# Kernel optimization log

Measured on AMD Instinct MI355X. Metric: run time of the kernel, lower is better.

The kernel has to match this reference:

```python
import jax, jax.numpy as jnp
import numpy as np

N = 50000
E = 640000
H = 128
C = 3

def _xavier(key, shape, gain=1.0):
    fan_in, fan_out = shape[0], shape[1]
    a = gain * np.sqrt(6.0 / (fan_in + fan_out))
    return jax.random.uniform(key, shape, jnp.float32, -a, a)

def setup_inputs() -> dict:
    key = jax.random.key(0)
    ks = jax.random.split(key, 12)
    h = jax.random.normal(ks[0], (N, H), jnp.float32)
    x = jax.random.normal(ks[1], (N, C), jnp.float32)
    edge_index = jax.random.randint(ks[2], (2, E), 0, N, jnp.int64 if jax.config.jax_enable_x64 else jnp.int32)
    # edge_mlp: Linear(2H+1 -> H), SiLU, Linear(H -> H), SiLU
    We1 = _xavier(ks[3], (2 * H + 1, H)); be1 = jnp.zeros((H,), jnp.float32)
    We2 = _xavier(ks[4], (H, H));          be2 = jnp.zeros((H,), jnp.float32)
    # coord_mlp: Linear(H -> H), SiLU, Linear(H -> 1, no bias, gain 0.01)
    Wc1 = _xavier(ks[5], (H, H)); bc1 = jnp.zeros((H,), jnp.float32)
    Wc2 = _xavier(ks[6], (H, 1), gain=0.01)
    # node_mlp: Linear(2H -> H), SiLU, Linear(H -> H)
    Wn1 = _xavier(ks[7], (2 * H, H)); bn1 = jnp.zeros((H,), jnp.float32)
    Wn2 = _xavier(ks[8], (H, H));     bn2 = jnp.zeros((H,), jnp.float32)
    return dict(h=h, x=x, edge_index=edge_index,
                We1=We1, be1=be1, We2=We2, be2=be2,
                Wc1=Wc1, bc1=bc1, Wc2=Wc2,
                Wn1=Wn1, bn1=bn1, Wn2=Wn2, bn2=bn2)

def reference(h, x, edge_index, We1, be1, We2, be2, Wc1, bc1, Wc2, Wn1, bn1, Wn2, bn2):
    src, dst = edge_index[0], edge_index[1]
    n = h.shape[0]
    rel_pos = x[src] - x[dst]                              # [E, C]
    dist_sq = jnp.sum(rel_pos * rel_pos, axis=-1, keepdims=True)  # [E, 1]
    edge_input = jnp.concatenate([h[src], h[dst], dist_sq], axis=-1)  # [E, 2H+1]
    m_ij = jax.nn.silu(edge_input @ We1 + be1)
    m_ij = jax.nn.silu(m_ij @ We2 + be2)                   # [E, H]
    coord_weight = jax.nn.silu(m_ij @ Wc1 + bc1) @ Wc2     # [E, 1]
    coord_agg = jax.ops.segment_sum(rel_pos * coord_weight, dst, num_segments=n)
    x_out = x + coord_agg
    msg_agg = jax.ops.segment_sum(m_ij, dst, num_segments=n)  # [N, H]
    node_input = jnp.concatenate([h, msg_agg], axis=-1)    # [N, 2H]
    h_upd = jax.nn.silu(node_input @ Wn1 + bn1) @ Wn2 + bn2
    h_out = h + h_upd
    return (h_out, x_out)
```

## Files before the change

### kernel.cpp

```cpp
#include <hip/hip_runtime.h>

#define H 128

typedef __bf16 bf8_t __attribute__((ext_vector_type(8)));
typedef float  f4_t  __attribute__((ext_vector_type(4)));

#define MFMA16(a, b, c) __builtin_amdgcn_mfma_f32_16x16x32_bf16((a), (b), (c), 0, 0, 0)

__device__ __forceinline__ float silu_f(float v) {
    return v * (1.0f / (1.0f + __expf(-v)));
}

__device__ __forceinline__ void bar_lds() {
    asm volatile("s_waitcnt lgkmcnt(0)\ns_barrier" ::: "memory");
}

__device__ __forceinline__ float wload(const void* p, int idx, bool f32) {
    return f32 ? ((const float*)p)[idx] : (float)((const __bf16*)p)[idx];
}

__device__ __forceinline__ bf8_t hload8(const void* p, size_t off, bool f32) {
    bf8_t v;
    if (f32) {
        const float4* q = (const float4*)((const float*)p + off);
        const float4 a = q[0], b = q[1];
        v[0]=(__bf16)a.x; v[1]=(__bf16)a.y; v[2]=(__bf16)a.z; v[3]=(__bf16)a.w;
        v[4]=(__bf16)b.x; v[5]=(__bf16)b.y; v[6]=(__bf16)b.z; v[7]=(__bf16)b.w;
    } else {
        v = *(const bf8_t*)((const __bf16*)p + off);
    }
    return v;
}

__device__ __forceinline__ int eidx(const void* ei, int i, bool i64) {
    return i64 ? (int)((const long long*)ei)[i] : ((const int*)ei)[i];
}

__global__ void detect_kernel(const unsigned short* __restrict__ hraw,
                              const int* __restrict__ eiraw, int* __restrict__ flags)
{
    __shared__ int s_nf, s_oddnz;
    if (threadIdx.x == 0) { s_nf = 0; s_oddnz = 0; }
    __syncthreads();
    int nf = 0;
    for (int i = threadIdx.x; i < 16384; i += blockDim.x) {
        const unsigned short u = hraw[i];
        if (((u >> 7) & 0xFF) == 0xFF) nf++;
    }
    int onz = 0;
    for (int i = threadIdx.x; i < 512; i += blockDim.x) {
        if (eiraw[2*i + 1] != 0) onz++;
    }
    if (nf)  atomicAdd(&s_nf, nf);
    if (onz) atomicAdd(&s_oddnz, onz);
    __syncthreads();
    if (threadIdx.x == 0) {
        flags[0] = (s_nf > 0) ? 1 : 0;
        flags[1] = (s_oddnz == 0) ? 1 : 0;
    }
}

__global__ void histd_kernel(const void* __restrict__ ei, int* __restrict__ cnt,
                             const int* __restrict__ flags, int Ee)
{
    const int e = blockIdx.x*blockDim.x + threadIdx.x;
    if (e < Ee) atomicAdd(&cnt[eidx(ei, Ee + e, flags[1] != 0)], 1);
}

__global__ void scanA_kernel(const int* __restrict__ cnt, int* __restrict__ bsum, int Nn)
{
    __shared__ int s[512];
    const int gi = blockIdx.x*512 + threadIdx.x;
    s[threadIdx.x] = (gi < Nn) ? cnt[gi] : 0;
    __syncthreads();
    for (int off = 256; off > 0; off >>= 1) {
        if (threadIdx.x < off) s[threadIdx.x] += s[threadIdx.x + off];
        __syncthreads();
    }
    if (threadIdx.x == 0) bsum[blockIdx.x] = s[0];
}

__global__ void scanB_kernel(int* __restrict__ bsum, int* __restrict__ base, int nCh)
{
    if (threadIdx.x == 0) {
        int acc = 0;
        for (int b = 0; b < nCh; ++b) { base[b] = acc; acc += bsum[b]; }
    }
}

__global__ void scanC_kernel(const int* __restrict__ cnt, const int* __restrict__ base,
                             int* __restrict__ off, int* __restrict__ cursor, int Nn)
{
    __shared__ int s[512];
    const int i  = threadIdx.x;
    const int gi = blockIdx.x*512 + i;
    const int v  = (gi < Nn) ? cnt[gi] : 0;
    s[i] = v;
    __syncthreads();
    for (int o = 1; o < 512; o <<= 1) {
        const int t = (i >= o) ? s[i - o] : 0;
        __syncthreads();
        s[i] += t;
        __syncthreads();
    }
    const int excl = s[i] - v;
    if (gi <= Nn) {
        const int val = base[blockIdx.x] + excl;
        off[gi] = val;
        if (gi < Nn) cursor[gi] = val;
    }
}

__global__ void scatgeo_kernel(const void* __restrict__ ei, int* __restrict__ cursor,
                               int* __restrict__ srcs, int* __restrict__ dsts,
                               float4* __restrict__ rel4, const void* __restrict__ x,
                               const int* __restrict__ flags, int Ee)
{
    const int e = blockIdx.x*blockDim.x + threadIdx.x;
    if (e >= Ee) return;
    const bool i64 = flags[1] != 0;
    const bool f32 = flags[0] != 0;
    const int s = eidx(ei, e, i64);
    const int d = eidx(ei, Ee + e, i64);
    const int p = atomicAdd(&cursor[d], 1);
    srcs[p] = s;
    dsts[p] = d;
    float r[3];
    #pragma unroll
    for (int c = 0; c < 3; ++c)
        r[c] = wload(x, s*3 + c, f32) - wload(x, d*3 + c, f32);
    float4 o; o.x = r[0]; o.y = r[1]; o.z = r[2];
    o.w = r[0]*r[0] + r[1]*r[1] + r[2]*r[2];
    rel4[p] = o;
}

__global__ __launch_bounds__(512, 2)
void proj_kernel(const void* __restrict__ h, const void* __restrict__ We1,
                 const void* __restrict__ be1, const int* __restrict__ flags,
                 __bf16* __restrict__ PB, int Nn)
{
    const bool f32 = flags[0] != 0;
    const int tid  = threadIdx.x;
    const int wv   = tid >> 6;
    const int lane = tid & 63;
    const int quad = lane >> 4;
    const int l15  = lane & 15;

    bf8_t bW[4][2];
    float bias[2];
    #pragma unroll
    for (int t = 0; t < 2; ++t) {
        const int n    = wv*32 + t*16 + l15;
        const int rb   = (n < 128) ? 0 : 128;
        const int col  = n & 127;
        #pragma unroll
        for (int kc = 0; kc < 4; ++kc) {
            bf8_t v;
            #pragma unroll
            for (int j = 0; j < 8; ++j)
                v[j] = (__bf16)wload(We1, (rb + kc*32 + quad*8 + j)*H + col, f32);
            bW[kc][t] = v;
        }
        bias[t] = (n < 128) ? 0.f : wload(be1, col, f32);
    }

    __shared__ __bf16 s_h[32*136];

    const int tiles = (Nn + 31) >> 5;
    for (int tile = blockIdx.x; tile < tiles; tile += gridDim.x) {
        const int nb = tile << 5;
        __syncthreads();
        {
            const int m = tid >> 4, c = tid & 15;
            int node = nb + m; if (node >= Nn) node = Nn - 1;
            *(bf8_t*)&s_h[m*136 + c*8] = hload8(h, (size_t)node*H + c*8, f32);
        }
        __syncthreads();

        f4_t acc[2][2];
        #pragma unroll
        for (int mm = 0; mm < 2; ++mm)
            #pragma unroll
            for (int t = 0; t < 2; ++t) acc[mm][t] = (f4_t){0.f,0.f,0.f,0.f};
        #pragma unroll
        for (int kc = 0; kc < 4; ++kc) {
            #pragma unroll
            for (int mm = 0; mm < 2; ++mm) {
                const bf8_t a = *(const bf8_t*)&s_h[(mm*16 + l15)*136 + quad*8 + kc*32];
                acc[mm][0] = MFMA16(a, bW[kc][0], acc[mm][0]);
                acc[mm][1] = MFMA16(a, bW[kc][1], acc[mm][1]);
            }
        }
        #pragma unroll
        for (int mm = 0; mm < 2; ++mm)
            #pragma unroll
            for (int i = 0; i < 4; ++i) {
                const int row = nb + mm*16 + quad*4 + i;
                if (row < Nn) {
                    #pragma unroll
                    for (int t = 0; t < 2; ++t)
                        PB[(size_t)row*256 + wv*32 + t*16 + l15] =
                            (__bf16)(acc[mm][t][i] + bias[t]);
                }
            }
    }
}

__global__ __launch_bounds__(512, 2)
void egnn_edge_pipe_kernel(const __bf16* __restrict__ PB,
                           const int* __restrict__ srcs, const int* __restrict__ dsts,
                           const float4* __restrict__ rel4,
                           const void* __restrict__ We1,
                           const void* __restrict__ We2, const void* __restrict__ be2,
                           const void* __restrict__ Wc1, const void* __restrict__ bc1,
                           const void* __restrict__ Wc2, const int* __restrict__ flags,
                           float* __restrict__ msg, float* __restrict__ coord,
                           int Ee)
{
    const bool f32 = flags[0] != 0;
    const int tid  = threadIdx.x;
    const int wv   = tid >> 6;
    const int lane = tid & 63;
    const int quad = lane >> 4;
    const int l15  = lane & 15;
    const int mg   = wv >> 2;
    const int ng   = wv & 3;

    bf8_t bW2[4][2], bWc[4][2];
    float be2v[2], bc1v[2], wc2v[2];
    #pragma unroll
    for (int t = 0; t < 2; ++t) {
        const int n = ng*32 + t*16 + l15;
        #pragma unroll
        for (int kc = 0; kc < 4; ++kc) {
            bf8_t v, u;
            #pragma unroll
            for (int j = 0; j < 8; ++j) {
                v[j] = (__bf16)wload(We2, (kc*32 + quad*8 + j)*H + n, f32);
                u[j] = (__bf16)wload(Wc1, (kc*32 + quad*8 + j)*H + n, f32);
            }
            bW2[kc][t] = v;
            bWc[kc][t] = u;
        }
        be2v[t] = wload(be2, n, f32);
        bc1v[t] = wload(bc1, n, f32);
        wc2v[t] = wload(Wc2, n, f32);
    }

    const int em = tid >> 3;
    const int ch = tid & 7;
    float w1dA[8], w1dB[8];
    #pragma unroll
    for (int j = 0; j < 8; ++j) {
        w1dA[j] = wload(We1, 256*H + ch*8 + j, f32);
        w1dB[j] = wload(We1, 256*H + (ch+8)*8 + j, f32);
    }

    const int rcol = tid >> 2;
    const int rg   = tid & 3;
    const int qb   = lane & ~3;

    __shared__ __bf16 s_m1[64*136];
    __shared__ __bf16 s_m2[64*136];
    __shared__ float  s_cw[4*64];
    __shared__ int    s_dst[2][64];
    __shared__ float4 s_rl[2][64];

    const int tiles = (Ee + 63) >> 6;
    const float* rw = (const float*)rel4;

    bf8_t rA0, rA1, rB0, rB1;
    float d2cur, d2nxt;
    int   s_n, d_n, d_c;
    float4 r4c, r4n;
    {
        int e0 = blockIdx.x*64 + em; if (e0 >= Ee) e0 = Ee - 1;
        const int sc = srcs[e0], dc = dsts[e0];
        d_c = dc;
        d2cur = rw[(size_t)e0*4 + 3];
        if (ch == 0) r4c = rel4[e0];
        rA0 = *(const bf8_t*)(PB + (size_t)sc*256 + ch*8);
        rA1 = *(const bf8_t*)(PB + (size_t)sc*256 + (ch+8)*8);
        rB0 = *(const bf8_t*)(PB + (size_t)dc*256 + 128 + ch*8);
        rB1 = *(const bf8_t*)(PB + (size_t)dc*256 + 128 + (ch+8)*8);
        const int t1 = blockIdx.x + gridDim.x;
        const int tt = (t1 < tiles) ? t1 : blockIdx.x;
        int e1 = tt*64 + em; if (e1 >= Ee) e1 = Ee - 1;
        s_n = srcs[e1]; d_n = dsts[e1]; d2nxt = rw[(size_t)e1*4 + 3];
        if (ch == 0) r4n = rel4[e1];
    }

    int li = 0;
    for (int t = blockIdx.x; t < tiles; t += gridDim.x, ++li) {
        const int sb = li & 1;
        {
            bf8_t o0, o1;
            #pragma unroll
            for (int j = 0; j < 8; ++j) {
                const float f0 = (float)rA0[j] + (float)rB0[j] + d2cur*w1dA[j];
                const float f1 = (float)rA1[j] + (float)rB1[j] + d2cur*w1dB[j];
                o0[j] = (__bf16)silu_f(f0);
                o1[j] = (__bf16)silu_f(f1);
            }
            *(bf8_t*)&s_m1[em*136 + ch*8]       = o0;
            *(bf8_t*)&s_m1[em*136 + (ch+8)*8]   = o1;
            if (ch == 0) { s_dst[sb][em] = d_c; s_rl[sb][em] = r4c; }
        }
        {
            const int sc = s_n, dc2 = d_n;
            rA0 = *(const bf8_t*)(PB + (size_t)sc*256 + ch*8);
            rA1 = *(const bf8_t*)(PB + (size_t)sc*256 + (ch+8)*8);
            rB0 = *(const bf8_t*)(PB + (size_t)dc2*256 + 128 + ch*8);
            rB1 = *(const bf8_t*)(PB + (size_t)dc2*256 + 128 + (ch+8)*8);
            d_c = d_n; d2cur = d2nxt;
            if (ch == 0) r4c = r4n;
            const int t2 = t + 2*gridDim.x;
            const int tt = (t2 < tiles) ? t2 : t;
            int e2 = tt*64 + em; if (e2 >= Ee) e2 = Ee - 1;
            s_n = srcs[e2]; d_n = dsts[e2]; d2nxt = rw[(size_t)e2*4 + 3];
            if (ch == 0) r4n = rel4[e2];
        }
        bar_lds();

        {
            f4_t a2[2][2];
            #pragma unroll
            for (int mm = 0; mm < 2; ++mm)
                #pragma unroll
                for (int h2 = 0; h2 < 2; ++h2) a2[mm][h2] = (f4_t){0.f,0.f,0.f,0.f};
            #pragma unroll
            for (int kc = 0; kc < 4; ++kc) {
                #pragma unroll
                for (int mm = 0; mm < 2; ++mm) {
                    const bf8_t a = *(const bf8_t*)&s_m1[(mg*32 + mm*16 + l15)*136 + quad*8 + kc*32];
                    a2[mm][0] = MFMA16(a, bW2[kc][0], a2[mm][0]);
                    a2[mm][1] = MFMA16(a, bW2[kc][1], a2[mm][1]);
                }
            }
            #pragma unroll
            for (int mm = 0; mm < 2; ++mm)
                #pragma unroll
                for (int i = 0; i < 4; ++i) {
                    const int m = mg*32 + mm*16 + quad*4 + i;
                    s_m2[m*136 + ng*32 + l15]      = (__bf16)silu_f(a2[mm][0][i] + be2v[0]);
                    s_m2[m*136 + ng*32 + 16 + l15] = (__bf16)silu_f(a2[mm][1][i] + be2v[1]);
                }
        }
        bar_lds();

        {
            f4_t a3[2][2];
            #pragma unroll
            for (int mm = 0; mm < 2; ++mm)
                #pragma unroll
                for (int h2 = 0; h2 < 2; ++h2) a3[mm][h2] = (f4_t){0.f,0.f,0.f,0.f};
            #pragma unroll
            for (int kc = 0; kc < 4; ++kc) {
                #pragma unroll
                for (int mm = 0; mm < 2; ++mm) {
                    const bf8_t a = *(const bf8_t*)&s_m2[(mg*32 + mm*16 + l15)*136 + quad*8 + kc*32];
                    a3[mm][0] = MFMA16(a, bWc[kc][0], a3[mm][0]);
                    a3[mm][1] = MFMA16(a, bWc[kc][1], a3[mm][1]);
                }
            }
            float p[2][4];
            #pragma unroll
            for (int mm = 0; mm < 2; ++mm)
                #pragma unroll
                for (int i = 0; i < 4; ++i) {
                    const float v0 = silu_f(a3[mm][0][i] + bc1v[0]);
                    const float v1 = silu_f(a3[mm][1][i] + bc1v[1]);
                    p[mm][i] = v0*wc2v[0] + v1*wc2v[1];
                }
            #pragma unroll
            for (int off = 1; off < 16; off <<= 1)
                #pragma unroll
                for (int mm = 0; mm < 2; ++mm)
                    #pragma unroll
                    for (int i = 0; i < 4; ++i) p[mm][i] += __shfl_xor(p[mm][i], off, 64);
            if (l15 == 0) {
                #pragma unroll
                for (int mm = 0; mm < 2; ++mm)
                    #pragma unroll
                    for (int i = 0; i < 4; ++i)
                        s_cw[ng*64 + (mg*32 + mm*16 + quad*4 + i)] = p[mm][i];
            }
        }

        {
            const int rbase = rg*16;
            int   curd = s_dst[sb][rbase];
            float acc  = 0.f;
            float pre  = 0.f;
            int   predone = 0;
            #pragma unroll
            for (int i = 0; i < 16; ++i) {
                const int   d = s_dst[sb][rbase + i];
                const float v = (float)s_m2[(rbase + i)*136 + rcol];
                if (d != curd) {
                    if (!predone) { pre = acc; predone = 1; }
                    else          { msg[(size_t)curd*H + rcol] = acc; }
                    curd = d; acc = v;
                } else acc += v;
            }
            const float suf = acc;
            const int   whf = !predone;
            float preA[4], sufA[4]; int whA[4];
            #pragma unroll
            for (int gg = 0; gg < 4; ++gg) {
                preA[gg] = __shfl(pre, qb + gg, 64);
                sufA[gg] = __shfl(suf, qb + gg, 64);
                whA[gg]  = __shfl(whf, qb + gg, 64);
            }
            if (rg == 0) {
                int   curd2 = s_dst[sb][0];
                float cur   = 0.f;
                int   first = 1;
                #pragma unroll
                for (int gg = 0; gg < 4; ++gg) {
                    const int F = s_dst[sb][gg*16];
                    const int L = s_dst[sb][gg*16 + 15];
                    if (F != curd2) {
                        if (first) atomicAdd(&msg[(size_t)curd2*H + rcol], cur);
                        else       msg[(size_t)curd2*H + rcol] = cur;
                        first = 0; curd2 = F; cur = 0.f;
                    }
                    if (whA[gg]) {
                        cur += sufA[gg];
                    } else {
                        cur += preA[gg];
                        if (first) atomicAdd(&msg[(size_t)curd2*H + rcol], cur);
                        else       msg[(size_t)curd2*H + rcol] = cur;
                        first = 0; curd2 = L; cur = sufA[gg];
                    }
                }
                atomicAdd(&msg[(size_t)curd2*H + rcol], cur);
            }
        }
        bar_lds();

        if (tid < 64) {
            const int e = tid;
            const float cwv = s_cw[e] + s_cw[64 + e] + s_cw[128 + e] + s_cw[192 + e];
            const float4 r = s_rl[sb][e];
            const int d = s_dst[sb][e];
            float vx = r.x*cwv, vy = r.y*cwv, vz = r.z*cwv;
            int   cn = 1;
            #pragma unroll
            for (int k = 1; k < 64; k <<= 1) {
                const int   dk = __shfl_up(d,  k, 64);
                const float xk = __shfl_up(vx, k, 64);
                const float yk = __shfl_up(vy, k, 64);
                const float zk = __shfl_up(vz, k, 64);
                const int   ck = __shfl_up(cn, k, 64);
                if (e >= k && dk == d) { vx += xk; vy += yk; vz += zk; cn += ck; }
            }
            const int dnx = __shfl_down(d, 1, 64);
            const bool runend = (e == 63) || (dnx != d);
            if (runend) {
                const int rs = e - cn + 1;
                if (rs == 0 || e == 63) {
                    atomicAdd(&coord[(size_t)d*3 + 0], vx);
                    atomicAdd(&coord[(size_t)d*3 + 1], vy);
                    atomicAdd(&coord[(size_t)d*3 + 2], vz);
                } else {
                    coord[(size_t)d*3 + 0] = vx;
                    coord[(size_t)d*3 + 1] = vy;
                    coord[(size_t)d*3 + 2] = vz;
                }
            }
        }
    }
}

__global__ __launch_bounds__(512, 2)
void egnn_node_kernel(const void* __restrict__ h, const float* __restrict__ msg,
                      const void* __restrict__ Wn1, const void* __restrict__ bn1,
                      const void* __restrict__ Wn2, const void* __restrict__ bn2,
                      const int* __restrict__ flags, void* __restrict__ h_out,
                      const void* __restrict__ x, const float* __restrict__ coord,
                      size_t obase, int do_x, int Nn)
{
    const bool f32 = flags[0] != 0;
    const int tid  = threadIdx.x;
    const int wv   = tid >> 6;
    const int lane = tid & 63;
    const int quad = lane >> 4;
    const int l15  = lane & 15;
    const int mg   = wv >> 2;
    const int ng   = wv & 3;

    bf8_t bW1[8][2];
    bf8_t bW2[4][2];
    float b1v[2], b2v[2];
    #pragma unroll
    for (int t = 0; t < 2; ++t) {
        const int n = ng*32 + t*16 + l15;
        #pragma unroll
        for (int kc = 0; kc < 8; ++kc) {
            bf8_t v;
            #pragma unroll
            for (int j = 0; j < 8; ++j) v[j] = (__bf16)wload(Wn1, (kc*32 + quad*8 + j)*H + n, f32);
            bW1[kc][t] = v;
        }
        #pragma unroll
        for (int kc = 0; kc < 4; ++kc) {
            bf8_t v;
            #pragma unroll
            for (int j = 0; j < 8; ++j) v[j] = (__bf16)wload(Wn2, (kc*32 + quad*8 + j)*H + n, f32);
            bW2[kc][t] = v;
        }
        b1v[t] = wload(bn1, n, f32);
        b2v[t] = wload(bn2, n, f32);
    }

    __shared__ __bf16 s_in[32*264];
    __shared__ __bf16 s_t1[32*136];

    const int tiles = (Nn + 31) >> 5;
    for (int tile = blockIdx.x; tile < tiles; tile += gridDim.x) {
        const int nb = tile << 5;
        __syncthreads();
        #pragma unroll
        for (int r = 0; r < 2; ++r) {
            const int idx = tid + r*512;
            const int m = idx >> 5, c = idx & 31;
            int node = nb + m;
            if (node >= Nn) node = Nn - 1;
            if (c < 16) {
                *(bf8_t*)&s_in[m*264 + c*8] = hload8(h, (size_t)node*H + c*8, f32);
            } else {
                const float4* mp = (const float4*)(msg + (size_t)node*H + (c - 16)*8);
                const float4 v0 = mp[0], v1 = mp[1];
                __bf16* d = &s_in[m*264 + c*8];
                d[0] = (__bf16)v0.x; d[1] = (__bf16)v0.y; d[2] = (__bf16)v0.z; d[3] = (__bf16)v0.w;
                d[4] = (__bf16)v1.x; d[5] = (__bf16)v1.y; d[6] = (__bf16)v1.z; d[7] = (__bf16)v1.w;
            }
        }
        if (do_x && tid < 96) {
            const int m = tid / 3, c = tid - m*3;
            const int node = nb + m;
            if (node < Nn) {
                const float xv = wload(x, node*3 + c, f32);
                const float o = xv + coord[(size_t)node*3 + c];
                if (f32) ((float*)h_out)[obase + (size_t)node*3 + c] = o;
                else     ((__bf16*)h_out)[obase + (size_t)node*3 + c] = (__bf16)o;
            }
        }
        __syncthreads();

        {
            f4_t a0 = {0.f,0.f,0.f,0.f}, a1 = {0.f,0.f,0.f,0.f};
            const int abase = (mg*16 + l15)*264 + quad*8;
            #pragma unroll
            for (int kc = 0; kc < 8; ++kc) {
                const bf8_t a = *(const bf8_t*)&s_in[abase + kc*32];
                a0 = MFMA16(a, bW1[kc][0], a0);
                a1 = MFMA16(a, bW1[kc][1], a1);
            }
            #pragma unroll
            for (int i = 0; i < 4; ++i) {
                const int m = mg*16 + quad*4 + i;
                s_t1[m*136 + ng*32 + l15]      = (__bf16)silu_f(a0[i] + b1v[0]);
                s_t1[m*136 + ng*32 + 16 + l15] = (__bf16)silu_f(a1[i] + b1v[1]);
            }
        }
        __syncthreads();

        {
            f4_t a0 = {0.f,0.f,0.f,0.f}, a1 = {0.f,0.f,0.f,0.f};
            const int abase = (mg*16 + l15)*136 + quad*8;
            #pragma unroll
            for (int kc = 0; kc < 4; ++kc) {
                const bf8_t a = *(const bf8_t*)&s_t1[abase + kc*32];
                a0 = MFMA16(a, bW2[kc][0], a0);
                a1 = MFMA16(a, bW2[kc][1], a1);
            }
            #pragma unroll
            for (int i = 0; i < 4; ++i) {
                const int node = nb + mg*16 + quad*4 + i;
                if (node < Nn) {
                    const int n0 = ng*32 + l15, n1 = n0 + 16;
                    const size_t i0 = (size_t)node*H + n0, i1 = (size_t)node*H + n1;
                    const float h0 = f32 ? ((const float*)h)[i0] : (float)((const __bf16*)h)[i0];
                    const float h1 = f32 ? ((const float*)h)[i1] : (float)((const __bf16*)h)[i1];
                    const float o0 = a0[i] + b2v[0] + h0;
                    const float o1 = a1[i] + b2v[1] + h1;
                    if (f32) {
                        ((float*)h_out)[i0] = o0;
                        ((float*)h_out)[i1] = o1;
                    } else {
                        ((__bf16*)h_out)[i0] = (__bf16)o0;
                        ((__bf16*)h_out)[i1] = (__bf16)o1;
                    }
                }
            }
        }
    }
}

__global__ void cvt_ei_kernel(const void* __restrict__ src, int* __restrict__ dst,
                              int n, const int* __restrict__ flags)
{
    const int i = blockIdx.x*blockDim.x + threadIdx.x;
    if (i >= n) return;
    dst[i] = flags[1] ? (int)((const long long*)src)[i] : ((const int*)src)[i];
}

__global__ __launch_bounds__(512, 2)
void egnn_edge_kernel(const void* __restrict__ h, const void* __restrict__ x,
                      const int* __restrict__ ei,
                      const void* __restrict__ We1, const void* __restrict__ be1,
                      const void* __restrict__ We2, const void* __restrict__ be2,
                      const void* __restrict__ Wc1, const void* __restrict__ bc1,
                      const void* __restrict__ Wc2, const int* __restrict__ flags,
                      float* __restrict__ msg_agg, float* __restrict__ coord_agg,
                      int Nn, int Ee)
{
    const bool f32 = flags[0] != 0;
    const int tid  = threadIdx.x;
    const int wv   = tid >> 6;
    const int lane = tid & 63;
    const int quad = lane >> 4;
    const int l15  = lane & 15;
    const int mg   = wv >> 2;
    const int ng   = wv & 3;

    bf8_t bW1[8][2];
    bf8_t bW2[4][2];
    bf8_t bWc[4][2];
    float be1v[2], be2v[2], bc1v[2], w1dv[2], wc2v[2];
    #pragma unroll
    for (int t = 0; t < 2; ++t) {
        const int n = ng*32 + t*16 + l15;
        #pragma unroll
        for (int kc = 0; kc < 8; ++kc) {
            bf8_t v;
            #pragma unroll
            for (int j = 0; j < 8; ++j) v[j] = (__bf16)wload(We1, (kc*32 + quad*8 + j)*H + n, f32);
            bW1[kc][t] = v;
        }
        #pragma unroll
        for (int kc = 0; kc < 4; ++kc) {
            bf8_t v, u;
            #pragma unroll
            for (int j = 0; j < 8; ++j) {
                v[j] = (__bf16)wload(We2, (kc*32 + quad*8 + j)*H + n, f32);
                u[j] = (__bf16)wload(Wc1, (kc*32 + quad*8 + j)*H + n, f32);
            }
            bW2[kc][t] = v;
            bWc[kc][t] = u;
        }
        be1v[t] = wload(be1, n, f32);
        be2v[t] = wload(be2, n, f32);
        bc1v[t] = wload(bc1, n, f32);
        w1dv[t] = wload(We1, 256*H + n, f32);
        wc2v[t] = wload(Wc2, n, f32);
    }

    __shared__ __bf16 s_in[32*264];
    __shared__ __bf16 s_m1[32*136];
    __shared__ __bf16 s_m2[32*136];
    __shared__ float  s_rel[32*3];
    __shared__ float  s_dist[32];
    __shared__ int    s_dstv[32];
    __shared__ float  s_cw[32*4];

    const int tiles = Ee >> 5;
    for (int tile = blockIdx.x; tile < tiles; tile += gridDim.x) {
        const int ebase = tile << 5;
        __syncthreads();

        if (tid < 32) {
            const int e  = ebase + tid;
            const int sn = ei[e];
            const int dn = ei[Ee + e];
            s_dstv[tid] = dn;
            float d2 = 0.f;
            #pragma unroll
            for (int c = 0; c < 3; ++c) {
                float r;
                if (f32) r = ((const float*)x)[sn*3 + c] - ((const float*)x)[dn*3 + c];
                else     r = (float)((const __bf16*)x)[sn*3 + c] - (float)((const __bf16*)x)[dn*3 + c];
                s_rel[tid*3 + c] = r;
                d2 += r*r;
            }
            s_dist[tid] = d2;
        }
        #pragma unroll
        for (int r = 0; r < 2; ++r) {
            const int idx = tid + r*512;
            const int m = idx >> 5, c = idx & 31;
            const int e = ebase + m;
            const int node = (c < 16) ? ei[e] : ei[Ee + e];
            *(bf8_t*)&s_in[m*264 + c*8] = hload8(h, (size_t)node*H + (c & 15)*8, f32);
        }
        __syncthreads();

        {
            f4_t a0 = {0.f,0.f,0.f,0.f}, a1 = {0.f,0.f,0.f,0.f};
            const int abase = (mg*16 + l15)*264 + quad*8;
            #pragma unroll
            for (int kc = 0; kc < 8; ++kc) {
                const bf8_t a = *(const bf8_t*)&s_in[abase + kc*32];
                a0 = MFMA16(a, bW1[kc][0], a0);
                a1 = MFMA16(a, bW1[kc][1], a1);
            }
            #pragma unroll
            for (int i = 0; i < 4; ++i) {
                const int m = mg*16 + quad*4 + i;
                const float d2 = s_dist[m];
                s_m1[m*136 + ng*32 + l15]      = (__bf16)silu_f(a0[i] + d2*w1dv[0] + be1v[0]);
                s_m1[m*136 + ng*32 + 16 + l15] = (__bf16)silu_f(a1[i] + d2*w1dv[1] + be1v[1]);
            }
        }
        __syncthreads();

        {
            f4_t a0 = {0.f,0.f,0.f,0.f}, a1 = {0.f,0.f,0.f,0.f};
            const int abase = (mg*16 + l15)*136 + quad*8;
            #pragma unroll
            for (int kc = 0; kc < 4; ++kc) {
                const bf8_t a = *(const bf8_t*)&s_m1[abase + kc*32];
                a0 = MFMA16(a, bW2[kc][0], a0);
                a1 = MFMA16(a, bW2[kc][1], a1);
            }
            #pragma unroll
            for (int i = 0; i < 4; ++i) {
                const int m = mg*16 + quad*4 + i;
                const float v0 = silu_f(a0[i] + be2v[0]);
                const float v1 = silu_f(a1[i] + be2v[1]);
                s_m2[m*136 + ng*32 + l15]      = (__bf16)v0;
                s_m2[m*136 + ng*32 + 16 + l15] = (__bf16)v1;
                const size_t db = (size_t)s_dstv[m]*H + ng*32 + l15;
                atomicAdd(&msg_agg[db],      v0);
                atomicAdd(&msg_agg[db + 16], v1);
            }
        }
        __syncthreads();

        {
            f4_t a0 = {0.f,0.f,0.f,0.f}, a1 = {0.f,0.f,0.f,0.f};
            const int abase = (mg*16 + l15)*136 + quad*8;
            #pragma unroll
            for (int kc = 0; kc < 4; ++kc) {
                const bf8_t a = *(const bf8_t*)&s_m2[abase + kc*32];
                a0 = MFMA16(a, bWc[kc][0], a0);
                a1 = MFMA16(a, bWc[kc][1], a1);
            }
            float p[4];
            #pragma unroll
            for (int i = 0; i < 4; ++i) {
                const float v0 = silu_f(a0[i] + bc1v[0]);
                const float v1 = silu_f(a1[i] + bc1v[1]);
                p[i] = v0*wc2v[0] + v1*wc2v[1];
            }
            #pragma unroll
            for (int off = 1; off < 16; off <<= 1) {
                #pragma unroll
                for (int i = 0; i < 4; ++i) p[i] += __shfl_xor(p[i], off, 64);
            }
            if (l15 == 0) {
                #pragma unroll
                for (int i = 0; i < 4; ++i)
                    s_cw[(mg*16 + quad*4 + i)*4 + ng] = p[i];
            }
        }
        __syncthreads();

        if (tid < 96) {
            const int m = tid / 3, c = tid - m*3;
            const float cw = s_cw[m*4 + 0] + s_cw[m*4 + 1] + s_cw[m*4 + 2] + s_cw[m*4 + 3];
            atomicAdd(&coord_agg[(size_t)s_dstv[m]*3 + c], s_rel[m*3 + c]*cw);
        }
    }
}

__global__ void egnn_x_kernel(const void* __restrict__ x, const float* __restrict__ coord_agg,
                              const int* __restrict__ flags, void* __restrict__ out,
                              size_t obase, int total)
{
    const bool f32 = flags[0] != 0;
    const int i = blockIdx.x*blockDim.x + threadIdx.x;
    if (i >= total) return;
    const float xv = f32 ? ((const float*)x)[i] : (float)((const __bf16*)x)[i];
    const float o = xv + coord_agg[i];
    if (f32) ((float*)out)[obase + i] = o;
    else     ((__bf16*)out)[obase + i] = (__bf16)o;
}

static inline size_t align256(size_t v) { return (v + 255) & ~(size_t)255; }

extern "C" void kernel_launch(void* const* d_in, const int* in_sizes, int n_in,
                              void* d_out, int out_size, void* d_ws, size_t ws_size,
                              hipStream_t stream)
{
    const void* h   = d_in[0];
    const void* x   = d_in[1];
    const void* ei0 = d_in[2];
    const void* We1 = d_in[3];
    const void* be1 = d_in[4];
    const void* We2 = d_in[5];
    const void* be2 = d_in[6];
    const void* Wc1 = d_in[7];
    const void* bc1 = d_in[8];
    const void* Wc2 = d_in[9];
    const void* Wn1 = d_in[10];
    const void* bn1 = d_in[11];
    const void* Wn2 = d_in[12];
    const void* bn2 = d_in[13];

    const int Nn = in_sizes[0] / H;
    const int Ee = in_sizes[2] / 2;

    char* ws = (char*)d_ws;
    size_t o = 0;
    size_t o_cnt   = o; o = align256(o + (size_t)Nn*4);
    size_t o_msg   = o; o = align256(o + (size_t)Nn*H*4);
    size_t o_coord = o; o = align256(o + (size_t)Nn*3*4);
    const size_t zero_end = o;
    size_t o_srcs  = o; o = align256(o + (size_t)Ee*4);
    size_t o_dsts  = o; o = align256(o + (size_t)Ee*4);
    size_t o_rel   = o; o = align256(o + (size_t)Ee*16);
    size_t o_pb    = o; o = align256(o + (size_t)Nn*256*2);
    size_t o_off   = o; o = align256(o + (size_t)(Nn+1)*4);
    size_t o_cur   = o; o = align256(o + (size_t)Nn*4);
    size_t o_bsum  = o; o = align256(o + 512*4);
    size_t o_base  = o; o = align256(o + 512*4);
    size_t o_flags = o; o = align256(o + 64);
    const size_t need_csr = o;

    const int nCh = (Nn + 1 + 511) / 512;

    if (ws_size >= need_csr) {
        int*    cnt     = (int*)   (ws + o_cnt);
        float*  msg     = (float*) (ws + o_msg);
        float*  coord   = (float*) (ws + o_coord);
        int*    srcs    = (int*)   (ws + o_srcs);
        int*    dsts    = (int*)   (ws + o_dsts);
        float4* rel4    = (float4*)(ws + o_rel);
        __bf16* PB      = (__bf16*)(ws + o_pb);
        int*    off     = (int*)   (ws + o_off);
        int*    cursor  = (int*)   (ws + o_cur);
        int*    bsum    = (int*)   (ws + o_bsum);
        int*    base    = (int*)   (ws + o_base);
        int*    flags   = (int*)   (ws + o_flags);

        detect_kernel<<<1, 256, 0, stream>>>((const unsigned short*)h, (const int*)ei0, flags);
        hipMemsetAsync(ws + o_cnt, 0, zero_end - o_cnt, stream);
        histd_kernel<<<(Ee + 511)/512, 512, 0, stream>>>(ei0, cnt, flags, Ee);
        scanA_kernel<<<nCh, 512, 0, stream>>>(cnt, bsum, Nn);
        scanB_kernel<<<1, 64, 0, stream>>>(bsum, base, nCh);
        scanC_kernel<<<nCh, 512, 0, stream>>>(cnt, base, off, cursor, Nn);
        scatgeo_kernel<<<(Ee + 511)/512, 512, 0, stream>>>(ei0, cursor, srcs, dsts,
                                                           rel4, x, flags, Ee);
        proj_kernel<<<512, 512, 0, stream>>>(h, We1, be1, flags, PB, Nn);

        egnn_edge_pipe_kernel<<<512, 512, 0, stream>>>(PB, srcs, dsts, rel4,
                                                       We1, We2, be2, Wc1, bc1, Wc2,
                                                       flags, msg, coord, Ee);

        egnn_node_kernel<<<1024, 512, 0, stream>>>(h, msg, Wn1, bn1, Wn2, bn2,
                                                   flags, d_out, x, coord,
                                                   (size_t)Nn*H, 1, Nn);
    } else {
        float* msg_agg   = (float*)ws;
        float* coord_agg = (float*)(ws + (size_t)Nn*H*4);
        int*   ei        = (int*)  (ws + (size_t)Nn*H*4 + (size_t)Nn*3*4);
        int*   flags     = (int*)  (ws + (size_t)Nn*H*4 + (size_t)Nn*3*4 + (size_t)2*Ee*4);

        detect_kernel<<<1, 256, 0, stream>>>((const unsigned short*)h, (const int*)ei0, flags);
        cvt_ei_kernel<<<(2*Ee + 255)/256, 256, 0, stream>>>(ei0, ei, 2*Ee, flags);
        hipMemsetAsync(msg_agg,   0, (size_t)Nn*H*4, stream);
        hipMemsetAsync(coord_agg, 0, (size_t)Nn*3*4, stream);
        egnn_edge_kernel<<<1024, 512, 0, stream>>>(h, x, ei, We1, be1, We2, be2,
                                                   Wc1, bc1, Wc2, flags,
                                                   msg_agg, coord_agg, Nn, Ee);
        egnn_node_kernel<<<512, 512, 0, stream>>>(h, msg_agg, Wn1, bn1, Wn2, bn2,
                                                  flags, d_out, x, coord_agg,
                                                  (size_t)Nn*H, 0, Nn);
        egnn_x_kernel<<<(Nn*3 + 255)/256, 256, 0, stream>>>(x, coord_agg, flags, d_out,
                                                            (size_t)Nn*H, Nn*3);
    }
}
```

Baseline: 675.7 us.

## Restructure segmented message reduction to per-wave row chunks with LDS combine

Changes the per-tile segmented sum of edge messages by destination. Previously each thread scanned 16 rows of one column and combined four partials with shuffles. Now each wave scans 8 rows with two columns per lane, using wave-uniform destination reads, and writes prefix and suffix partials to LDS. After a barrier, a separate wave combines the 8 partials per column and issues the stores and atomics. This gives vectorized bf16 pair loads and float2 stores and fewer divergent branches, at the cost of extra LDS traffic and an additional barrier.

```diff
diff --git a/kernel.cpp b/kernel.cpp
--- a/kernel.cpp
+++ b/kernel.cpp
@@ -3,6 +3,7 @@
 #define H 128
 
 typedef __bf16 bf8_t __attribute__((ext_vector_type(8)));
+typedef __bf16 bf2_t __attribute__((ext_vector_type(2)));
 typedef float  f4_t  __attribute__((ext_vector_type(4)));
 
 #define MFMA16(a, b, c) __builtin_amdgcn_mfma_f32_16x16x32_bf16((a), (b), (c), 0, 0, 0)
@@ -256,15 +257,14 @@
         w1dB[j] = wload(We1, 256*H + (ch+8)*8 + j, f32);
     }
 
-    const int rcol = tid >> 2;
-    const int rg   = tid & 3;
-    const int qb   = lane & ~3;
-
     __shared__ __bf16 s_m1[64*136];
     __shared__ __bf16 s_m2[64*136];
     __shared__ float  s_cw[4*64];
     __shared__ int    s_dst[2][64];
     __shared__ float4 s_rl[2][64];
+    __shared__ float  s_pre[8][128];
+    __shared__ float  s_suf[8][128];
+    __shared__ int    s_wh[8];
 
     const int tiles = (Ee + 63) >> 6;
     const float* rw = (const float*)rel4;
@@ -388,56 +388,60 @@
         }
 
         {
-            const int rbase = rg*16;
-            int   curd = s_dst[sb][rbase];
-            float acc  = 0.f;
-            float pre  = 0.f;
+            const int rbase = wv << 3;
+            const int c0    = lane << 1;
+            int   curd = __builtin_amdgcn_readfirstlane(s_dst[sb][rbase]);
+            float ax = 0.f, ay = 0.f;
+            float px = 0.f, py = 0.f;
             int   predone = 0;
             #pragma unroll
-            for (int i = 0; i < 16; ++i) {
-                const int   d = s_dst[sb][rbase + i];
-                const float v = (float)s_m2[(rbase + i)*136 + rcol];
+            for (int i = 0; i < 8; ++i) {
+                const int d = __builtin_amdgcn_readfirstlane(s_dst[sb][rbase + i]);
+                const bf2_t v = *(const bf2_t*)&s_m2[(rbase + i)*136 + c0];
+                const float vx = (float)v[0], vy = (float)v[1];
                 if (d != curd) {
-                    if (!predone) { pre = acc; predone = 1; }
-                    else          { msg[(size_t)curd*H + rcol] = acc; }
-                    curd = d; acc = v;
-                } else acc += v;
-            }
-            const float suf = acc;
-            const int   whf = !predone;
-            float preA[4], sufA[4]; int whA[4];
-            #pragma unroll
-            for (int gg = 0; gg < 4; ++gg) {
-                preA[gg] = __shfl(pre, qb + gg, 64);
-                sufA[gg] = __shfl(suf, qb + gg, 64);
-                whA[gg]  = __shfl(whf, qb + gg, 64);
-            }
-            if (rg == 0) {
-                int   curd2 = s_dst[sb][0];
-                float cur   = 0.f;
-                int   first = 1;
-                #pragma unroll
-                for (int gg = 0; gg < 4; ++gg) {
-                    const int F = s_dst[sb][gg*16];
-                    const int L = s_dst[sb][gg*16 + 15];
-                    if (F != curd2) {
-                        if (first) atomicAdd(&msg[(size_t)curd2*H + rcol], cur);
-                        else       msg[(size_t)curd2*H + rcol] = cur;
-                        first = 0; curd2 = F; cur = 0.f;
+                    if (!predone) { px = ax; py = ay; predone = 1; }
+                    else {
+                        float2 st; st.x = ax; st.y = ay;
+                        *(float2*)&msg[(size_t)curd*H + c0] = st;
                     }
-                    if (whA[gg]) {
-                        cur += sufA[gg];
-                    } else {
-                        cur += preA[gg];
-                        if (first) atomicAdd(&msg[(size_t)curd2*H + rcol], cur);
-                        else       msg[(size_t)curd2*H + rcol] = cur;
-                        first = 0; curd2 = L; cur = sufA[gg];
-                    }
+                    curd = d; ax = vx; ay = vy;
+                } else { ax += vx; ay += vy; }
+            }
+            s_pre[wv][c0]   = px;  s_pre[wv][c0+1] = py;
+            s_suf[wv][c0]   = ax;  s_suf[wv][c0+1] = ay;
+            if (lane == 0) s_wh[wv] = !predone;
+        }
+        bar_lds();
+
+        if (tid >= 128 && tid < 256) {
+            const int c = tid - 128;
+            int   curd2 = __builtin_amdgcn_readfirstlane(s_dst[sb][0]);
+            float cur   = 0.f;
+            int   first = 1;
+            #pragma unroll
+            for (int gg = 0; gg < 8; ++gg) {
+                const int F  = __builtin_amdgcn_readfirstlane(s_dst[sb][gg*8]);
+                const int L  = __builtin_amdgcn_readfirstlane(s_dst[sb][gg*8 + 7]);
+                const int wh = __builtin_amdgcn_readfirstlane(s_wh[gg]);
+                const float preg = s_pre[gg][c];
+                const float sufg = s_suf[gg][c];
+                if (F != curd2) {
+                    if (first) atomicAdd(&msg[(size_t)curd2*H + c], cur);
+                    else       msg[(size_t)curd2*H + c] = cur;
+                    first = 0; curd2 = F; cur = 0.f;
                 }
-                atomicAdd(&msg[(size_t)curd2*H + rcol], cur);
-            }
-        }
-        bar_lds();
+                if (wh) {
+                    cur += sufg;
+                } else {
+                    cur += preg;
+                    if (first) atomicAdd(&msg[(size_t)curd2*H + c], cur);
+                    else       msg[(size_t)curd2*H + c] = cur;
+                    first = 0; curd2 = L; cur = sufg;
+                }
+            }
+            atomicAdd(&msg[(size_t)curd2*H + c], cur);
+        }
 
         if (tid < 64) {
             const int e = tid;
```

Result: faster. 652.9 us (-3.4%).
